# Kernel tuning notes

Measured on AMD Instinct MI355X. Metric: run time of the kernel, lower is better.

Reference implementation:

```python
import jax, jax.numpy as jnp
import numpy as np

EPS = 1e-6
SEARCH_RANGE = 4  # K = 2*R+1 = 9


def setup_inputs() -> dict:
    key = jax.random.key(0)
    k1, k2, k3, k4 = jax.random.split(key, 4)
    B, C, H, W = 4, 128, 128, 240
    E = 64
    F_L = jax.random.normal(k1, (B, C, H, W), dtype=jnp.float32)
    F_R = jax.random.normal(k2, (B, C, H, W), dtype=jnp.float32)
    d0 = jax.random.uniform(k3, (B, 1, H, W), dtype=jnp.float32) * 64.0  # pixel disparity
    phi_w = jax.random.normal(k4, (E, C), dtype=jnp.float32) / np.sqrt(C)  # 1x1 conv weight
    return {"F_L": F_L, "F_R": F_R, "d0": d0, "phi_w": phi_w}


def _embed(x, phi_w):
    # 1x1 conv + channel L2 normalize (cosine embedding)
    y = jnp.einsum('ec,bchw->behw', phi_w, x)
    norm = jnp.sqrt(jnp.sum(y * y, axis=1, keepdims=True)) + EPS
    return y / norm


def reference(F_L, F_R, d0, phi_w):
    R = SEARCH_RANGE
    FL = _embed(F_L, phi_w)  # (B,E,H,W)
    FR = _embed(F_R, phi_w)
    B, E, H, W = FL.shape
    deltas = jnp.arange(-R, R + 1, dtype=FL.dtype)  # (K,)
    xx = jnp.arange(W, dtype=FL.dtype)  # base x grid
    # x' = x - (d0 + delta); align_corners=True grid round-trips to pixel coords exactly,
    # y coordinate is identity, so warp is 1D bilinear along W with border clamp.
    xprime = xx[None, None, None, :] - d0[:, None, 0, :, :] - deltas[None, :, None, None]  # (B,K,H,W)
    x0 = jnp.floor(xprime)
    w = xprime - x0  # bilinear weight
    i0 = jnp.clip(x0.astype(jnp.int32), 0, W - 1)
    i1 = jnp.clip(x0.astype(jnp.int32) + 1, 0, W - 1)
    FR_e = FR[:, None]  # (B,1,E,H,W)
    g0 = jnp.take_along_axis(FR_e, i0[:, :, None, :, :], axis=4)  # (B,K,E,H,W)
    g1 = jnp.take_along_axis(FR_e, i1[:, :, None, :, :], axis=4)
    FR_s = g0 * (1.0 - w)[:, :, None] + g1 * w[:, :, None]
    cost_vol = jnp.einsum('behw,bkehw->bkhw', FL, FR_s)  # (B,K,H,W)
    return cost_vol
```

## Files before the change

### kernel.cpp

```cpp
#include <hip/hip_runtime.h>
#include <hip/hip_bf16.h>

#define NB 4
#define NC 128
#define NH 128
#define NW 240
#define NE 64
#define NK 9
#define PLANE (NH*NW)
#define CHW (NC*PLANE)
#define XS 244

typedef __attribute__((ext_vector_type(8))) short short8;
typedef __attribute__((ext_vector_type(4))) float f32x4;
typedef __attribute__((ext_vector_type(2))) __fp16 fp16x2;
typedef __attribute__((ext_vector_type(8))) __fp16 fp16x8;

__device__ __forceinline__ unsigned pkh(float x, float y){
  fp16x2 h = __builtin_amdgcn_cvt_pkrtz(x, y);
  return __builtin_bit_cast(unsigned, h);
}
__device__ __forceinline__ float fdot2u(unsigned a, unsigned b, float c){
#if __has_builtin(__builtin_amdgcn_fdot2)
  return __builtin_amdgcn_fdot2(__builtin_bit_cast(fp16x2,a),
                                __builtin_bit_cast(fp16x2,b), c, false);
#else
  fp16x2 ha = __builtin_bit_cast(fp16x2,a), hb = __builtin_bit_cast(fp16x2,b);
  return c + (float)ha[0]*(float)hb[0] + (float)ha[1]*(float)hb[1];
#endif
}
__device__ __forceinline__ int swz(int r){ return (r ^ (r>>3)) & 7; }

__global__ __launch_bounds__(1024, 4)
void fused_kernel(const float* __restrict__ xL,
                  const float* __restrict__ xR,
                  const float* __restrict__ d0g,
                  const float* __restrict__ phig,
                  float* __restrict__ outg)
{
  __shared__ __attribute__((aligned(16))) unsigned short xs[NC*XS];
  __shared__ __attribute__((aligned(16))) unsigned short phis[NE*136];
  __shared__ __attribute__((aligned(16))) unsigned short FLb[NW*64];

  const int tid  = threadIdx.x;
  const int lane = tid & 63;
  const int wv   = tid >> 6;
  const int b    = blockIdx.x >> 7;
  const int h    = blockIdx.x & 127;
  const size_t base = (size_t)b*CHW + (size_t)h*NW;
  const int pixbase = (b*NH + h)*NW;

  float d0v = (tid < 960) ? d0g[pixbase + (tid >> 2)] : 0.f;

  float4 xr[8];
  #pragma unroll
  for (int i = 0; i < 7; ++i) {
    unsigned idx = i*1024 + tid;
    unsigned c = idx / 60u, s = idx - 60u*c;
    xr[i] = *(const float4*)(xL + base + (size_t)c*PLANE + 4*s);
  }
  if (tid < 512) {
    unsigned idx = 7168 + tid;
    unsigned c = idx / 60u, s = idx - 60u*c;
    xr[7] = *(const float4*)(xL + base + (size_t)c*PLANE + 4*s);
  }
  float4 pr[2];
  #pragma unroll
  for (int i = 0; i < 2; ++i) {
    int idx = i*1024 + tid;
    pr[i] = *(const float4*)(phig + (idx>>5)*128 + 4*(idx&31));
  }
  #pragma unroll
  for (int i = 0; i < 2; ++i) {
    int idx = i*1024 + tid;
    uint2 pk; pk.x = pkh(pr[i].x, pr[i].y); pk.y = pkh(pr[i].z, pr[i].w);
    *(uint2*)&phis[(idx>>5)*136 + 4*(idx&31)] = pk;
  }
  #pragma unroll
  for (int i = 0; i < 7; ++i) {
    unsigned idx = i*1024 + tid;
    unsigned c = idx / 60u, s = idx - 60u*c;
    uint2 pk; pk.x = pkh(xr[i].x, xr[i].y); pk.y = pkh(xr[i].z, xr[i].w);
    *(uint2*)&xs[c*XS + 4*s] = pk;
  }
  if (tid < 512) {
    unsigned idx = 7168 + tid;
    unsigned c = idx / 60u, s = idx - 60u*c;
    uint2 pk; pk.x = pkh(xr[7].x, xr[7].y); pk.y = pkh(xr[7].z, xr[7].w);
    *(uint2*)&xs[c*XS + 4*s] = pk;
  }
  __syncthreads();

  float4 xrR[8];
  #pragma unroll
  for (int i = 0; i < 7; ++i) {
    unsigned idx = i*1024 + tid;
    unsigned c = idx / 60u, s = idx - 60u*c;
    xrR[i] = *(const float4*)(xR + base + (size_t)c*PLANE + 4*s);
  }
  if (tid < 512) {
    unsigned idx = 7168 + tid;
    unsigned c = idx / 60u, s = idx - 60u*c;
    xrR[7] = *(const float4*)(xR + base + (size_t)c*PLANE + 4*s);
  }

  const int mrow = lane & 15;
  const int kg   = lane >> 4;
  const int nt   = wv;
  const int n    = 16*nt + mrow;

  uint2 flpk[4];
  {
    f32x4 acc[4];
    #pragma unroll
    for (int mt = 0; mt < 4; ++mt) acc[mt] = (f32x4){0.f,0.f,0.f,0.f};
    if (nt < 15) {
      const int col = n;
      #pragma unroll
      for (int ks = 0; ks < 4; ++ks) {
        const int r0 = 32*ks + 8*kg;
        fp16x8 bv;
        #pragma unroll
        for (int j = 0; j < 8; ++j)
          bv[j] = *(const __fp16*)&xs[(r0 + j)*XS + col];
        #pragma unroll
        for (int mt = 0; mt < 4; ++mt) {
          short8 raw = *(const short8*)&phis[(16*mt + mrow)*136 + 32*ks + 8*kg];
          fp16x8 af = __builtin_bit_cast(fp16x8, raw);
          acc[mt] = __builtin_amdgcn_mfma_f32_16x16x32_f16(af, bv, acc[mt], 0, 0, 0);
        }
      }
      float ss = 0.f;
      #pragma unroll
      for (int mt = 0; mt < 4; ++mt)
        #pragma unroll
        for (int r = 0; r < 4; ++r)
          ss += acc[mt][r]*acc[mt][r];
      ss += __shfl_xor(ss, 16, 64);
      ss += __shfl_xor(ss, 32, 64);
      float inv = 1.f/(sqrtf(ss) + 1e-6f);
      #pragma unroll
      for (int mt = 0; mt < 4; ++mt) {
        flpk[mt].x = pkh(acc[mt][0]*inv, acc[mt][1]*inv);
        flpk[mt].y = pkh(acc[mt][2]*inv, acc[mt][3]*inv);
      }
    }
  }
  __syncthreads();

  if (nt < 15) {
    #pragma unroll
    for (int mt = 0; mt < 4; ++mt) {
      int e0 = 16*mt + 4*kg;
      int pos = n*64 + (((e0>>3) ^ swz(n))<<3) + (e0&7);
      *(uint2*)&FLb[pos] = flpk[mt];
    }
  }
  #pragma unroll
  for (int i = 0; i < 7; ++i) {
    unsigned idx = i*1024 + tid;
    unsigned c = idx / 60u, s = idx - 60u*c;
    uint2 pk; pk.x = pkh(xrR[i].x, xrR[i].y); pk.y = pkh(xrR[i].z, xrR[i].w);
    *(uint2*)&xs[c*XS + 4*s] = pk;
  }
  if (tid < 512) {
    unsigned idx = 7168 + tid;
    unsigned c = idx / 60u, s = idx - 60u*c;
    uint2 pk; pk.x = pkh(xrR[7].x, xrR[7].y); pk.y = pkh(xrR[7].z, xrR[7].w);
    *(uint2*)&xs[c*XS + 4*s] = pk;
  }
  __syncthreads();

  uint2 frpk[4];
  {
    f32x4 acc[4];
    #pragma unroll
    for (int mt = 0; mt < 4; ++mt) acc[mt] = (f32x4){0.f,0.f,0.f,0.f};
    if (nt < 15) {
      const int col = n;
      #pragma unroll
      for (int ks = 0; ks < 4; ++ks) {
        const int r0 = 32*ks + 8*kg;
        fp16x8 bv;
        #pragma unroll
        for (int j = 0; j < 8; ++j)
          bv[j] = *(const __fp16*)&xs[(r0 + j)*XS + col];
        #pragma unroll
        for (int mt = 0; mt < 4; ++mt) {
          short8 raw = *(const short8*)&phis[(16*mt + mrow)*136 + 32*ks + 8*kg];
          fp16x8 af = __builtin_bit_cast(fp16x8, raw);
          acc[mt] = __builtin_amdgcn_mfma_f32_16x16x32_f16(af, bv, acc[mt], 0, 0, 0);
        }
      }
      float ss = 0.f;
      #pragma unroll
      for (int mt = 0; mt < 4; ++mt)
        #pragma unroll
        for (int r = 0; r < 4; ++r)
          ss += acc[mt][r]*acc[mt][r];
      ss += __shfl_xor(ss, 16, 64);
      ss += __shfl_xor(ss, 32, 64);
      float inv = 1.f/(sqrtf(ss) + 1e-6f);
      #pragma unroll
      for (int mt = 0; mt < 4; ++mt) {
        frpk[mt].x = pkh(acc[mt][0]*inv, acc[mt][1]*inv);
        frpk[mt].y = pkh(acc[mt][2]*inv, acc[mt][3]*inv);
      }
    }
  }
  __syncthreads();

  unsigned short* FRb = &xs[0];
  if (nt < 15) {
    #pragma unroll
    for (int mt = 0; mt < 4; ++mt) {
      int e0 = 16*mt + 4*kg;
      int pos = n*64 + (((e0>>3) ^ swz(n))<<3) + (e0&7);
      *(uint2*)&FRb[pos] = frpk[mt];
    }
  }
  __syncthreads();

  float* cvb = (float*)phis;
  if (tid < 960) {
    const int p  = tid >> 2;
    const int eh = tid & 3;
    float xf  = (float)p - d0v;
    float x0  = floorf(xf);
    float wfr = xf - x0;
    int jb = (int)x0 - 4;

    unsigned fl[8];
    #pragma unroll
    for (int i = 0; i < 2; ++i) {
      int c4 = 2*eh + i;
      uint4 raw = *(const uint4*)&FLb[p*64 + ((c4 ^ swz(p))<<3)];
      fl[4*i+0]=raw.x; fl[4*i+1]=raw.y; fl[4*i+2]=raw.z; fl[4*i+3]=raw.w;
    }

    float D[10];
    #pragma unroll
    for (int t = 0; t < 10; ++t) {
      int j = jb + t;
      j = j < 0 ? 0 : (j > NW-1 ? NW-1 : j);
      float s = 0.f;
      #pragma unroll
      for (int i = 0; i < 2; ++i) {
        int c4 = 2*eh + i;
        uint4 raw = *(const uint4*)&FRb[j*64 + ((c4 ^ swz(j))<<3)];
        s = fdot2u(fl[4*i+0], raw.x, s);
        s = fdot2u(fl[4*i+1], raw.y, s);
        s = fdot2u(fl[4*i+2], raw.z, s);
        s = fdot2u(fl[4*i+3], raw.w, s);
      }
      D[t] = s;
    }
    #pragma unroll
    for (int t = 0; t < 10; ++t) {
      D[t] += __shfl_xor(D[t], 1, 64);
      D[t] += __shfl_xor(D[t], 2, 64);
    }

    #define WK(k) { const int t0 = 8-(k); cvb[(k)*NW + p] = (1.f - wfr)*D[t0] + wfr*D[t0+1]; }
    if      (eh == 0) { WK(0) WK(1) WK(2) }
    else if (eh == 1) { WK(3) WK(4) }
    else if (eh == 2) { WK(5) WK(6) }
    else              { WK(7) WK(8) }
    #undef WK
  }
  __syncthreads();

  if (tid < 540) {
    int k = tid/60, w4 = tid - 60*k;
    float4 v = *(const float4*)&cvb[k*NW + 4*w4];
    *(float4*)(outg + (size_t)b*NK*PLANE + (size_t)h*NW + (size_t)k*PLANE + 4*w4) = v;
  }
}

extern "C" void kernel_launch(void* const* d_in, const int* in_sizes, int n_in,
                              void* d_out, int out_size, void* d_ws, size_t ws_size,
                              hipStream_t stream) {
  const float* xL   = (const float*)d_in[0];
  const float* xR   = (const float*)d_in[1];
  const float* d0g  = (const float*)d_in[2];
  const float* phig = (const float*)d_in[3];
  float* outg = (float*)d_out;
  fused_kernel<<<dim3(NB*NH), dim3(1024), 0, stream>>>(xL, xR, d0g, phig, outg);
}
```

Before: 153.6 us.

## Stream input channels in two 64-channel chunks to halve LDS and raise occupancy

The 1x1-conv embedding GEMM for each image now runs in two 64-channel chunks instead of staging all 128 channels at once. The shared staging buffer shrinks to half, and the register prefetch buffer shrinks from eight float4 to four. The next chunk's global loads are issued before the current chunk's MFMA work, so loading overlaps compute. Lower LDS and register use, plus a raised launch-bounds occupancy hint, should let more blocks share a CU, at the cost of extra barriers.

```diff
diff --git a/kernel.cpp b/kernel.cpp
--- a/kernel.cpp
+++ b/kernel.cpp
@@ -31,14 +31,14 @@
 }
 __device__ __forceinline__ int swz(int r){ return (r ^ (r>>3)) & 7; }
 
-__global__ __launch_bounds__(1024, 4)
+__global__ __launch_bounds__(1024, 8)
 void fused_kernel(const float* __restrict__ xL,
                   const float* __restrict__ xR,
                   const float* __restrict__ d0g,
                   const float* __restrict__ phig,
                   float* __restrict__ outg)
 {
-  __shared__ __attribute__((aligned(16))) unsigned short xs[NC*XS];
+  __shared__ __attribute__((aligned(16))) unsigned short xs[64*XS];
   __shared__ __attribute__((aligned(16))) unsigned short phis[NE*136];
   __shared__ __attribute__((aligned(16))) unsigned short FLb[NW*64];
 
@@ -50,20 +50,71 @@
   const size_t base = (size_t)b*CHW + (size_t)h*NW;
   const int pixbase = (b*NH + h)*NW;
 
+  const int mrow = lane & 15;
+  const int kg   = lane >> 4;
+  const int nt   = wv;
+  const int n    = 16*nt + mrow;
+
   float d0v = (tid < 960) ? d0g[pixbase + (tid >> 2)] : 0.f;
 
-  float4 xr[8];
-  #pragma unroll
-  for (int i = 0; i < 7; ++i) {
-    unsigned idx = i*1024 + tid;
-    unsigned c = idx / 60u, s = idx - 60u*c;
-    xr[i] = *(const float4*)(xL + base + (size_t)c*PLANE + 4*s);
-  }
-  if (tid < 512) {
-    unsigned idx = 7168 + tid;
-    unsigned c = idx / 60u, s = idx - 60u*c;
-    xr[7] = *(const float4*)(xL + base + (size_t)c*PLANE + 4*s);
-  }
+  auto load_chunk = [&](const float* __restrict__ xg, int ch, float4 (&r)[4]) {
+    if (tid < 960) {
+      #pragma unroll
+      for (int i = 0; i < 4; ++i) {
+        unsigned idx = i*960 + tid;
+        unsigned c = idx / 60u, s = idx - 60u*c;
+        r[i] = *(const float4*)(xg + base + (size_t)(64*ch + c)*PLANE + 4*s);
+      }
+    }
+  };
+  auto write_chunk = [&](float4 (&r)[4]) {
+    if (tid < 960) {
+      #pragma unroll
+      for (int i = 0; i < 4; ++i) {
+        unsigned idx = i*960 + tid;
+        unsigned c = idx / 60u, s = idx - 60u*c;
+        uint2 pk; pk.x = pkh(r[i].x, r[i].y); pk.y = pkh(r[i].z, r[i].w);
+        *(uint2*)&xs[c*XS + 4*s] = pk;
+      }
+    }
+  };
+  auto gemm_chunk = [&](f32x4 (&acc)[4], int ch) {
+    if (nt < 15) {
+      #pragma unroll
+      for (int ks = 0; ks < 2; ++ks) {
+        const int r0 = 32*ks + 8*kg;
+        fp16x8 bv;
+        #pragma unroll
+        for (int j = 0; j < 8; ++j)
+          bv[j] = *(const __fp16*)&xs[(r0 + j)*XS + n];
+        #pragma unroll
+        for (int mt = 0; mt < 4; ++mt) {
+          short8 raw = *(const short8*)&phis[(16*mt + mrow)*136 + 64*ch + 32*ks + 8*kg];
+          fp16x8 af = __builtin_bit_cast(fp16x8, raw);
+          acc[mt] = __builtin_amdgcn_mfma_f32_16x16x32_f16(af, bv, acc[mt], 0, 0, 0);
+        }
+      }
+    }
+  };
+  auto norm_pack = [&](f32x4 (&acc)[4], uint2 (&pk)[4]) {
+    float ss = 0.f;
+    #pragma unroll
+    for (int mt = 0; mt < 4; ++mt)
+      #pragma unroll
+      for (int r = 0; r < 4; ++r)
+        ss += acc[mt][r]*acc[mt][r];
+    ss += __shfl_xor(ss, 16, 64);
+    ss += __shfl_xor(ss, 32, 64);
+    float inv = 1.f/(sqrtf(ss) + 1e-6f);
+    #pragma unroll
+    for (int mt = 0; mt < 4; ++mt) {
+      pk[mt].x = pkh(acc[mt][0]*inv, acc[mt][1]*inv);
+      pk[mt].y = pkh(acc[mt][2]*inv, acc[mt][3]*inv);
+    }
+  };
+
+  float4 st[4];
+  load_chunk(xL, 0, st);
   float4 pr[2];
   #pragma unroll
   for (int i = 0; i < 2; ++i) {
@@ -76,78 +127,23 @@
     uint2 pk; pk.x = pkh(pr[i].x, pr[i].y); pk.y = pkh(pr[i].z, pr[i].w);
     *(uint2*)&phis[(idx>>5)*136 + 4*(idx&31)] = pk;
   }
-  #pragma unroll
-  for (int i = 0; i < 7; ++i) {
-    unsigned idx = i*1024 + tid;
-    unsigned c = idx / 60u, s = idx - 60u*c;
-    uint2 pk; pk.x = pkh(xr[i].x, xr[i].y); pk.y = pkh(xr[i].z, xr[i].w);
-    *(uint2*)&xs[c*XS + 4*s] = pk;
-  }
-  if (tid < 512) {
-    unsigned idx = 7168 + tid;
-    unsigned c = idx / 60u, s = idx - 60u*c;
-    uint2 pk; pk.x = pkh(xr[7].x, xr[7].y); pk.y = pkh(xr[7].z, xr[7].w);
-    *(uint2*)&xs[c*XS + 4*s] = pk;
-  }
-  __syncthreads();
-
-  float4 xrR[8];
-  #pragma unroll
-  for (int i = 0; i < 7; ++i) {
-    unsigned idx = i*1024 + tid;
-    unsigned c = idx / 60u, s = idx - 60u*c;
-    xrR[i] = *(const float4*)(xR + base + (size_t)c*PLANE + 4*s);
-  }
-  if (tid < 512) {
-    unsigned idx = 7168 + tid;
-    unsigned c = idx / 60u, s = idx - 60u*c;
-    xrR[7] = *(const float4*)(xR + base + (size_t)c*PLANE + 4*s);
-  }
-
-  const int mrow = lane & 15;
-  const int kg   = lane >> 4;
-  const int nt   = wv;
-  const int n    = 16*nt + mrow;
-
+  write_chunk(st);
+  __syncthreads();
+
+  f32x4 accL[4];
+  #pragma unroll
+  for (int mt = 0; mt < 4; ++mt) accL[mt] = (f32x4){0.f,0.f,0.f,0.f};
+
+  load_chunk(xL, 1, st);
+  gemm_chunk(accL, 0);
+  __syncthreads();
+  write_chunk(st);
+  __syncthreads();
+
+  load_chunk(xR, 0, st);
+  gemm_chunk(accL, 1);
   uint2 flpk[4];
-  {
-    f32x4 acc[4];
-    #pragma unroll
-    for (int mt = 0; mt < 4; ++mt) acc[mt] = (f32x4){0.f,0.f,0.f,0.f};
-    if (nt < 15) {
-      const int col = n;
-      #pragma unroll
-      for (int ks = 0; ks < 4; ++ks) {
-        const int r0 = 32*ks + 8*kg;
-        fp16x8 bv;
-        #pragma unroll
-        for (int j = 0; j < 8; ++j)
-          bv[j] = *(const __fp16*)&xs[(r0 + j)*XS + col];
-        #pragma unroll
-        for (int mt = 0; mt < 4; ++mt) {
-          short8 raw = *(const short8*)&phis[(16*mt + mrow)*136 + 32*ks + 8*kg];
-          fp16x8 af = __builtin_bit_cast(fp16x8, raw);
-          acc[mt] = __builtin_amdgcn_mfma_f32_16x16x32_f16(af, bv, acc[mt], 0, 0, 0);
-        }
-      }
-      float ss = 0.f;
-      #pragma unroll
-      for (int mt = 0; mt < 4; ++mt)
-        #pragma unroll
-        for (int r = 0; r < 4; ++r)
-          ss += acc[mt][r]*acc[mt][r];
-      ss += __shfl_xor(ss, 16, 64);
-      ss += __shfl_xor(ss, 32, 64);
-      float inv = 1.f/(sqrtf(ss) + 1e-6f);
-      #pragma unroll
-      for (int mt = 0; mt < 4; ++mt) {
-        flpk[mt].x = pkh(acc[mt][0]*inv, acc[mt][1]*inv);
-        flpk[mt].y = pkh(acc[mt][2]*inv, acc[mt][3]*inv);
-      }
-    }
-  }
-  __syncthreads();
-
+  norm_pack(accL, flpk);
   if (nt < 15) {
     #pragma unroll
     for (int mt = 0; mt < 4; ++mt) {
@@ -156,58 +152,23 @@
       *(uint2*)&FLb[pos] = flpk[mt];
     }
   }
-  #pragma unroll
-  for (int i = 0; i < 7; ++i) {
-    unsigned idx = i*1024 + tid;
-    unsigned c = idx / 60u, s = idx - 60u*c;
-    uint2 pk; pk.x = pkh(xrR[i].x, xrR[i].y); pk.y = pkh(xrR[i].z, xrR[i].w);
-    *(uint2*)&xs[c*XS + 4*s] = pk;
-  }
-  if (tid < 512) {
-    unsigned idx = 7168 + tid;
-    unsigned c = idx / 60u, s = idx - 60u*c;
-    uint2 pk; pk.x = pkh(xrR[7].x, xrR[7].y); pk.y = pkh(xrR[7].z, xrR[7].w);
-    *(uint2*)&xs[c*XS + 4*s] = pk;
-  }
-  __syncthreads();
-
+  __syncthreads();
+  write_chunk(st);
+  __syncthreads();
+
+  f32x4 accR[4];
+  #pragma unroll
+  for (int mt = 0; mt < 4; ++mt) accR[mt] = (f32x4){0.f,0.f,0.f,0.f};
+
+  load_chunk(xR, 1, st);
+  gemm_chunk(accR, 0);
+  __syncthreads();
+  write_chunk(st);
+  __syncthreads();
+
+  gemm_chunk(accR, 1);
   uint2 frpk[4];
-  {
-    f32x4 acc[4];
-    #pragma unroll
-    for (int mt = 0; mt < 4; ++mt) acc[mt] = (f32x4){0.f,0.f,0.f,0.f};
-    if (nt < 15) {
-      const int col = n;
-      #pragma unroll
-      for (int ks = 0; ks < 4; ++ks) {
-        const int r0 = 32*ks + 8*kg;
-        fp16x8 bv;
-        #pragma unroll
-        for (int j = 0; j < 8; ++j)
-          bv[j] = *(const __fp16*)&xs[(r0 + j)*XS + col];
-        #pragma unroll
-        for (int mt = 0; mt < 4; ++mt) {
-          short8 raw = *(const short8*)&phis[(16*mt + mrow)*136 + 32*ks + 8*kg];
-          fp16x8 af = __builtin_bit_cast(fp16x8, raw);
-          acc[mt] = __builtin_amdgcn_mfma_f32_16x16x32_f16(af, bv, acc[mt], 0, 0, 0);
-        }
-      }
-      float ss = 0.f;
-      #pragma unroll
-      for (int mt = 0; mt < 4; ++mt)
-        #pragma unroll
-        for (int r = 0; r < 4; ++r)
-          ss += acc[mt][r]*acc[mt][r];
-      ss += __shfl_xor(ss, 16, 64);
-      ss += __shfl_xor(ss, 32, 64);
-      float inv = 1.f/(sqrtf(ss) + 1e-6f);
-      #pragma unroll
-      for (int mt = 0; mt < 4; ++mt) {
-        frpk[mt].x = pkh(acc[mt][0]*inv, acc[mt][1]*inv);
-        frpk[mt].y = pkh(acc[mt][2]*inv, acc[mt][3]*inv);
-      }
-    }
-  }
+  norm_pack(accR, frpk);
   __syncthreads();
 
   unsigned short* FRb = &xs[0];
```

After: 148.1 us. -3.6%, faster.
